# Performance work log

Hardware: AMD Instinct MI355X
Metric: run time of the kernel (lower is better)

## Reference

```python
import jax, jax.numpy as jnp
import numpy as np

N = 8192
E = 131072
IN = 512
H = 8
C = 128
HC = H * C
EPS = 1e-5
NEG_SLOPE = 0.2


def _gatv2(x, src, dst, Wl, bl, Wr, br, att, bias):
    """GATv2Conv (PyG semantics, concat=True, self-loops already in src/dst)."""
    n = x.shape[0]
    xl = (x @ Wl + bl).reshape(n, H, C)  # source transform (lin_l)
    xr = (x @ Wr + br).reshape(n, H, C)  # dest transform (lin_r)
    m = xl[src] + xr[dst]                # [E,H,C] per-edge message
    e = jnp.einsum('ehc,hc->eh', jax.nn.leaky_relu(m, NEG_SLOPE), att)  # [E,H]
    # segment softmax over destination nodes
    emax = jax.ops.segment_max(e, dst, num_segments=n)
    w = jnp.exp(e - emax[dst])
    denom = jax.ops.segment_sum(w, dst, num_segments=n)
    alpha = w / denom[dst]               # [E,H]
    out = jax.ops.segment_sum(alpha[:, :, None] * xl[src], dst, num_segments=n)
    return out.reshape(n, HC) + bias


def _bn(x, gamma, beta):
    mu = jnp.mean(x, axis=0)
    var = jnp.mean((x - mu) ** 2, axis=0)
    return (x - mu) * jax.lax.rsqrt(var + EPS) * gamma + beta


def setup_inputs() -> dict:
    key = jax.random.key(0)
    ks = jax.random.split(key, 16)
    s = 0.05
    return {
        'x': jax.random.normal(ks[0], (N, IN), jnp.float32),
        'edge_index': jax.random.randint(ks[1], (2, E), 0, N, jnp.int32),
        'W1l': jax.random.normal(ks[2], (IN, HC), jnp.float32) * s,
        'b1l': jnp.zeros((HC,), jnp.float32),
        'W1r': jax.random.normal(ks[3], (IN, HC), jnp.float32) * s,
        'b1r': jnp.zeros((HC,), jnp.float32),
        'att1': jax.random.normal(ks[4], (H, C), jnp.float32) * s,
        'bias1': jnp.zeros((HC,), jnp.float32),
        'g1': jnp.ones((HC,), jnp.float32),
        'beta1': jnp.zeros((HC,), jnp.float32),
        'W2l': jax.random.normal(ks[5], (HC, HC), jnp.float32) * s,
        'b2l': jnp.zeros((HC,), jnp.float32),
        'W2r': jax.random.normal(ks[6], (HC, HC), jnp.float32) * s,
        'b2r': jnp.zeros((HC,), jnp.float32),
        'att2': jax.random.normal(ks[7], (H, C), jnp.float32) * s,
        'bias2': jnp.zeros((HC,), jnp.float32),
        'g2': jnp.ones((HC,), jnp.float32),
        'beta2': jnp.zeros((HC,), jnp.float32),
    }


def reference(x, edge_index, W1l, b1l, W1r, b1r, att1, bias1, g1, beta1,
              W2l, b2l, W2r, b2r, att2, bias2, g2, beta2):
    n = x.shape[0]
    loops = jnp.arange(n, dtype=edge_index.dtype)
    src = jnp.concatenate([edge_index[0], loops])
    dst = jnp.concatenate([edge_index[1], loops])
    h = _gatv2(x, src, dst, W1l, b1l, W1r, b1r, att1, bias1)
    h = jax.nn.elu(_bn(h, g1, beta1))
    h = _gatv2(h, src, dst, W2l, b2l, W2r, b2r, att2, bias2)
    h = jax.nn.elu(_bn(h, g2, beta2))
    return h
```

## Files before the change

kernel.cpp:

```cpp
#include <hip/hip_runtime.h>
#include <stdint.h>

#define NN     8192
#define NEDGE  131072
#define NETOT  (NEDGE + NN)
#define K_IN   512
#define HC_    1024
#define NOUT   2048
#define BNEPS  1e-5f
#define SLOPE  0.2f

typedef __bf16 bf16x8 __attribute__((ext_vector_type(8)));
typedef float  f32x4  __attribute__((ext_vector_type(4)));
typedef float  f32x2  __attribute__((ext_vector_type(2)));

__device__ __forceinline__ float bf2f(unsigned short u) {
  union { uint32_t u; float f; } c; c.u = ((uint32_t)u) << 16; return c.f;
}
__device__ __forceinline__ unsigned short f2bf(float f) {
  union { float f; uint32_t u; } c; c.f = f;
  uint32_t r = c.u + 0x7fffu + ((c.u >> 16) & 1u);
  return (unsigned short)(r >> 16);
}
__device__ __forceinline__ f32x2 upk2(uint32_t u) {
  union { uint32_t u; float f; } a, b;
  a.u = u << 16; b.u = u & 0xffff0000u;
  f32x2 r; r.x = a.f; r.y = b.f; return r;
}

__device__ __forceinline__ void gload16(const void* g, void* l) {
  __builtin_amdgcn_global_load_lds(
      (const __attribute__((address_space(1))) uint32_t*)g,
      (__attribute__((address_space(3))) uint32_t*)l, 16, 0, 0);
}

#define SBAR() do { asm volatile("" ::: "memory"); __builtin_amdgcn_s_barrier(); asm volatile("" ::: "memory"); } while (0)

__global__ __launch_bounds__(256) void k_cvt_bf16(const float* __restrict__ in,
                                                  unsigned short* __restrict__ out, int n4) {
  int i = blockIdx.x * 256 + threadIdx.x;
  if (i >= n4) return;
  float4 v = *(const float4*)&in[(size_t)i * 4];
  ushort4 o;
  o.x = f2bf(v.x); o.y = f2bf(v.y); o.z = f2bf(v.z); o.w = f2bf(v.w);
  *(ushort4*)&out[(size_t)i * 4] = o;
}

__global__ __launch_bounds__(256) void k_transpose2_bf16(const float* __restrict__ Wa,
                                                         const float* __restrict__ Wb,
                                                         unsigned short* __restrict__ Wt,
                                                         int K, int N) {
  __shared__ float tile[32][33];
  const float* W = blockIdx.z ? Wb : Wa;
  unsigned short* dst = Wt + (size_t)blockIdx.z * N * K;
  int n0 = blockIdx.x * 32, k0 = blockIdx.y * 32;
  int tx = threadIdx.x & 31, ty = threadIdx.x >> 5;
  for (int i = ty; i < 32; i += 8)
    tile[i][tx] = W[(size_t)(k0 + i) * N + n0 + tx];
  __syncthreads();
  for (int i = ty; i < 32; i += 8)
    dst[(size_t)(n0 + i) * K + k0 + tx] = f2bf(tile[tx][i]);
}

__global__ __launch_bounds__(256) void k_hist(const int* __restrict__ ei, int* __restrict__ cnt) {
  int i = blockIdx.x * 256 + threadIdx.x;
  if (i >= NETOT) return;
  int d = (i < NEDGE) ? ei[NEDGE + i] : (i - NEDGE);
  atomicAdd(&cnt[d], 1);
}

__global__ __launch_bounds__(256) void k_scan(const int* __restrict__ cnt,
                                              int* __restrict__ rowptr,
                                              int* __restrict__ cursor) {
  __shared__ int part[256];
  int t = threadIdx.x;
  int base = t * 32;
  int s = 0;
  for (int i = 0; i < 32; ++i) s += cnt[base + i];
  part[t] = s;
  __syncthreads();
  for (int off = 1; off < 256; off <<= 1) {
    int u = (t >= off) ? part[t - off] : 0;
    __syncthreads();
    part[t] += u;
    __syncthreads();
  }
  int run = part[t] - s;
  for (int i = 0; i < 32; ++i) {
    rowptr[base + i] = run;
    cursor[base + i] = run;
    run += cnt[base + i];
  }
  if (t == 255) rowptr[NN] = run;
}

__global__ __launch_bounds__(256) void k_scatter(const int* __restrict__ ei,
                                                 int* __restrict__ cursor,
                                                 int* __restrict__ srcs) {
  int i = blockIdx.x * 256 + threadIdx.x;
  if (i >= NETOT) return;
  int s, d;
  if (i < NEDGE) { s = ei[i]; d = ei[NEDGE + i]; }
  else           { s = d = i - NEDGE; }
  int pos = atomicAdd(&cursor[d], 1);
  srcs[pos] = s;
}

__global__ __launch_bounds__(512, 2) void k_gemm256(const unsigned short* __restrict__ A,
                                                    const unsigned short* __restrict__ Bt,
                                                    const float* __restrict__ biasL,
                                                    const float* __restrict__ biasR,
                                                    unsigned short* __restrict__ C,
                                                    int K) {
  __shared__ unsigned short lA[2][256 * 64];
  __shared__ unsigned short lB[2][256 * 64];

  const int bid = blockIdx.x;
  const int xcd = bid & 7, idx = bid >> 3;
  const int m0 = (xcd * 4 + (idx & 3)) * 256;
  const int n0 = (idx >> 2) * 256;

  const int tid = threadIdx.x;
  const int l   = tid & 63;
  const int wv  = tid >> 6;
  const int wm  = wv >> 2, wn = wv & 3;
  const int l15 = l & 15, l4 = l >> 4;

  const int srow = tid >> 3;
  const int ssgk = (tid & 7) ^ (srow & 7);

  const f32x4 vzero = {0.f, 0.f, 0.f, 0.f};
  f32x4 acc[8][4];
#pragma unroll
  for (int i = 0; i < 8; ++i)
#pragma unroll
    for (int j = 0; j < 4; ++j) acc[i][j] = vzero;

  bf16x8 a2[8];
  bf16x8 bb[2][4];

  auto stageA = [&](int kt, int h) {
    const int buf = kt & 1;
    const size_t go = (size_t)(m0 + h * 128 + srow) * K + (size_t)kt * 64 + ssgk * 8;
    unsigned short* lp = &lA[buf][h * 8192 + tid * 8];
    gload16(&A[go], lp);
    gload16(&A[go + (size_t)64 * K], lp + 4096);
  };
  auto stageB = [&](int kt, int h) {
    const int buf = kt & 1;
    const size_t go = (size_t)(n0 + h * 128 + srow) * K + (size_t)kt * 64 + ssgk * 8;
    unsigned short* lp = &lB[buf][h * 8192 + tid * 8];
    gload16(&Bt[go], lp);
    gload16(&Bt[go + (size_t)64 * K], lp + 4096);
  };
  auto readA = [&](int buf, int qm) {
#pragma unroll
    for (int fm = 0; fm < 4; ++fm)
#pragma unroll
      for (int kk = 0; kk < 2; ++kk) {
        int r = wm * 128 + (qm * 4 + fm) * 16 + l15;
        int g = (kk * 4 + l4) ^ (r & 7);
        a2[fm * 2 + kk] = *(const bf16x8*)&lA[buf][r * 64 + g * 8];
      }
  };
  auto readB = [&](int buf, int qn) {
#pragma unroll
    for (int fn = 0; fn < 2; ++fn)
#pragma unroll
      for (int kk = 0; kk < 2; ++kk) {
        int r = wn * 64 + (qn * 2 + fn) * 16 + l15;
        int g = (kk * 4 + l4) ^ (r & 7);
        bb[qn][fn * 2 + kk] = *(const bf16x8*)&lB[buf][r * 64 + g * 8];
      }
  };
  auto quad = [&](int qm, int qn) {
    __builtin_amdgcn_s_setprio(1);
#pragma unroll
    for (int fm = 0; fm < 4; ++fm)
#pragma unroll
      for (int fn = 0; fn < 2; ++fn)
#pragma unroll
        for (int kk = 0; kk < 2; ++kk)
          acc[qm * 4 + fm][qn * 2 + fn] = __builtin_amdgcn_mfma_f32_16x16x32_bf16(
              a2[fm * 2 + kk], bb[qn][fn * 2 + kk], acc[qm * 4 + fm][qn * 2 + fn], 0, 0, 0);
    __builtin_amdgcn_s_setprio(0);
  };

  const int NT = K >> 6;

  stageA(0, 0); stageA(0, 1); stageB(0, 0); stageB(0, 1);
  if (NT > 1) stageA(1, 0);
  asm volatile("s_waitcnt vmcnt(2)" ::: "memory");
  SBAR();

  for (int t = 0; t < NT; ++t) {
    const int buf = t & 1;
    readA(buf, 0); readB(buf, 0);
    if (t + 1 < NT) stageA(t + 1, 1);
    SBAR();
    quad(0, 0);
    SBAR();
    readB(buf, 1);
    if (t + 1 < NT) stageB(t + 1, 0);
    SBAR();
    quad(0, 1);
    SBAR();
    readA(buf, 1);
    if (t + 1 < NT) stageB(t + 1, 1);
    SBAR();
    quad(1, 0);
    SBAR();
    if (t + 2 < NT) stageA(t + 2, 0);
    asm volatile("s_waitcnt vmcnt(2)" ::: "memory");
    SBAR();
    quad(1, 1);
    SBAR();
  }

  const float* bias = (n0 < HC_) ? biasL : (biasR - HC_);
#pragma unroll
  for (int fm = 0; fm < 8; ++fm) {
#pragma unroll
    for (int fn = 0; fn < 4; ++fn) {
      int col = n0 + wn * 64 + fn * 16 + l15;
      float bv = bias[col];
#pragma unroll
      for (int j = 0; j < 4; ++j) {
        int row = m0 + wm * 128 + fm * 16 + l4 * 4 + j;
        C[(size_t)row * NOUT + col] = f2bf(acc[fm][fn][j] + bv);
      }
    }
  }
}

template <bool OUT_BF16>
__global__ __launch_bounds__(256, 8) void k_edge_agg(const unsigned short* __restrict__ XLR,
                                                     const float* __restrict__ att,
                                                     const float* __restrict__ bias,
                                                     const int* __restrict__ rowptr,
                                                     const int* __restrict__ srcs,
                                                     void* __restrict__ outp) {
  const int tid  = threadIdx.x;
  const int wv   = tid >> 6;
  const int d    = blockIdx.x * 2 + (wv >> 1);
  const int half = wv & 1;
  const int l    = tid & 63;
  const int c0   = half * 512 + l * 8;

  f32x2 attv[4], xrv[4];
  {
    const f32x2* ap = (const f32x2*)&att[c0];
    attv[0] = ap[0]; attv[1] = ap[1]; attv[2] = ap[2]; attv[3] = ap[3];
    uint4 u = *(const uint4*)&XLR[(size_t)d * NOUT + HC_ + c0];
    xrv[0] = upk2(u.x); xrv[1] = upk2(u.y); xrv[2] = upk2(u.z); xrv[3] = upk2(u.w);
  }

  f32x2 acc0 = {0.f, 0.f}, acc1 = {0.f, 0.f}, acc2 = {0.f, 0.f}, acc3 = {0.f, 0.f};
  float den = 0.f;

  const int beg = __builtin_amdgcn_readfirstlane(rowptr[d]);
  const int end = __builtin_amdgcn_readfirstlane(rowptr[d + 1]);
  const int e1  = end - 1;

  auto rowp = [&](int s) { return (const uint4*)&XLR[(size_t)s * NOUT + c0]; };
  auto cl   = [&](int i) { return i < e1 ? i : e1; };

  uint4 R0 = *rowp(srcs[beg]);
  uint4 R1 = *rowp(srcs[cl(beg + 1)]);
  uint4 R2 = *rowp(srcs[cl(beg + 2)]);
  int sN1 = srcs[cl(beg + 3)];
  int sN2 = srcs[cl(beg + 4)];

  int i = beg;

#define STEP(R)                                                                \
  {                                                                            \
    f32x2 x0 = upk2(R.x), x1 = upk2(R.y), x2 = upk2(R.z), x3 = upk2(R.w);      \
    R = *rowp(sN1);                                                            \
    sN1 = sN2;                                                                 \
    sN2 = srcs[cl(i + 5)];                                                     \
    f32x2 ps = {0.f, 0.f}, y;                                                  \
    y = x0 + xrv[0]; ps = __builtin_elementwise_max(y, y * SLOPE) * attv[0] + ps; \
    y = x1 + xrv[1]; ps = __builtin_elementwise_max(y, y * SLOPE) * attv[1] + ps; \
    y = x2 + xrv[2]; ps = __builtin_elementwise_max(y, y * SLOPE) * attv[2] + ps; \
    y = x3 + xrv[3]; ps = __builtin_elementwise_max(y, y * SLOPE) * attv[3] + ps; \
    float p = ps.x + ps.y;                                                     \
    p += __shfl_xor(p, 1);                                                     \
    p += __shfl_xor(p, 2);                                                     \
    p += __shfl_xor(p, 4);                                                     \
    p += __shfl_xor(p, 8);                                                     \
    float wgt = __expf(p);                                                     \
    den += wgt;                                                                \
    f32x2 w2 = {wgt, wgt};                                                     \
    acc0 = w2 * x0 + acc0;                                                     \
    acc1 = w2 * x1 + acc1;                                                     \
    acc2 = w2 * x2 + acc2;                                                     \
    acc3 = w2 * x3 + acc3;                                                     \
    ++i;                                                                       \
  }

  while (true) {
    STEP(R0); if (i == end) break;
    STEP(R1); if (i == end) break;
    STEP(R2); if (i == end) break;
  }
#undef STEP

  const float inv = 1.0f / den;
  const f32x2* bp = (const f32x2*)&bias[c0];
  float o[8];
  o[0] = acc0.x * inv + bp[0].x; o[1] = acc0.y * inv + bp[0].y;
  o[2] = acc1.x * inv + bp[1].x; o[3] = acc1.y * inv + bp[1].y;
  o[4] = acc2.x * inv + bp[2].x; o[5] = acc2.y * inv + bp[2].y;
  o[6] = acc3.x * inv + bp[3].x; o[7] = acc3.y * inv + bp[3].y;

  if (OUT_BF16) {
    unsigned short* op = (unsigned short*)outp + (size_t)d * HC_ + c0;
    ushort4 u0, u1;
    u0.x = f2bf(o[0]); u0.y = f2bf(o[1]); u0.z = f2bf(o[2]); u0.w = f2bf(o[3]);
    u1.x = f2bf(o[4]); u1.y = f2bf(o[5]); u1.z = f2bf(o[6]); u1.w = f2bf(o[7]);
    *(ushort4*)&op[0] = u0;
    *(ushort4*)&op[4] = u1;
  } else {
    float* op = (float*)outp + (size_t)d * HC_ + c0;
    float4 v0 = {o[0], o[1], o[2], o[3]};
    float4 v1 = {o[4], o[5], o[6], o[7]};
    *(float4*)&op[0] = v0;
    *(float4*)&op[4] = v1;
  }
}

template <bool IN_BF16>
__global__ __launch_bounds__(256) void k_colstats(const void* __restrict__ Xp,
                                                  float* __restrict__ stats) {
  int col = blockIdx.x * 256 + threadIdx.x;
  int r0 = blockIdx.y * 128;
  float s = 0.f, q = 0.f;
  for (int r = r0; r < r0 + 128; ++r) {
    float v = IN_BF16 ? bf2f(((const unsigned short*)Xp)[(size_t)r * HC_ + col])
                      : ((const float*)Xp)[(size_t)r * HC_ + col];
    s += v;
    q += v * v;
  }
  atomicAdd(&stats[col], s);
  atomicAdd(&stats[HC_ + col], q);
}

template <bool IN_BF16, bool OUT_BF16>
__global__ __launch_bounds__(256) void k_bn_elu(const void* __restrict__ Xp,
                                                const float* __restrict__ stats,
                                                const float* __restrict__ gamma,
                                                const float* __restrict__ beta,
                                                void* __restrict__ outp) {
  size_t idx = (size_t)blockIdx.x * 256 + threadIdx.x;
  size_t e0 = idx * 4;
  int col = (int)(e0 & (HC_ - 1));
  float xs[4];
  if (IN_BF16) {
    ushort4 u = *(const ushort4*)&((const unsigned short*)Xp)[e0];
    xs[0] = bf2f(u.x); xs[1] = bf2f(u.y); xs[2] = bf2f(u.z); xs[3] = bf2f(u.w);
  } else {
    float4 xv = *(const float4*)&((const float*)Xp)[e0];
    xs[0] = xv.x; xs[1] = xv.y; xs[2] = xv.z; xs[3] = xv.w;
  }
  float os[4];
  const float rn = 1.0f / (float)NN;
#pragma unroll
  for (int j = 0; j < 4; ++j) {
    int c = col + j;
    float mu = stats[c] * rn;
    float var = stats[HC_ + c] * rn - mu * mu;
    float v = (xs[j] - mu) * rsqrtf(var + BNEPS) * gamma[c] + beta[c];
    os[j] = v > 0.f ? v : (__expf(v) - 1.f);
  }
  if (OUT_BF16) {
    ushort4 o;
    o.x = f2bf(os[0]); o.y = f2bf(os[1]); o.z = f2bf(os[2]); o.w = f2bf(os[3]);
    *(ushort4*)&((unsigned short*)outp)[e0] = o;
  } else {
    float4 o = {os[0], os[1], os[2], os[3]};
    *(float4*)&((float*)outp)[e0] = o;
  }
}

extern "C" void kernel_launch(void* const* d_in, const int* in_sizes, int n_in,
                              void* d_out, int out_size, void* d_ws, size_t ws_size,
                              hipStream_t stream) {
  const float* x     = (const float*)d_in[0];
  const int*   ei    = (const int*)d_in[1];
  const float* W1l   = (const float*)d_in[2];
  const float* b1l   = (const float*)d_in[3];
  const float* W1r   = (const float*)d_in[4];
  const float* b1r   = (const float*)d_in[5];
  const float* att1  = (const float*)d_in[6];
  const float* bias1 = (const float*)d_in[7];
  const float* g1    = (const float*)d_in[8];
  const float* be1   = (const float*)d_in[9];
  const float* W2l   = (const float*)d_in[10];
  const float* b2l   = (const float*)d_in[11];
  const float* W2r   = (const float*)d_in[12];
  const float* b2r   = (const float*)d_in[13];
  const float* att2  = (const float*)d_in[14];
  const float* bias2 = (const float*)d_in[15];
  const float* g2    = (const float*)d_in[16];
  const float* be2   = (const float*)d_in[17];
  float* out = (float*)d_out;

  char* wsb = (char*)d_ws;
  size_t o = 0;
  auto alloc = [&](size_t b) {
    void* p = wsb + o;
    o = (o + b + 255) & ~(size_t)255;
    return p;
  };
  unsigned short* xbf  = (unsigned short*)alloc((size_t)NN * K_IN * 2);
  unsigned short* wT1  = (unsigned short*)alloc((size_t)NOUT * K_IN * 2);
  unsigned short* wT2  = (unsigned short*)alloc((size_t)NOUT * HC_ * 2);
  unsigned short* XLR  = (unsigned short*)alloc((size_t)NN * NOUT * 2);
  unsigned short* h0   = (unsigned short*)alloc((size_t)NN * HC_ * 2);
  int* cnt     = (int*)alloc((size_t)NN * 4);
  int* rowptr  = (int*)alloc((size_t)(NN + 1) * 4);
  int* cursor  = (int*)alloc((size_t)NN * 4);
  int* srcs    = (int*)alloc((size_t)NETOT * 4);
  float* stats = (float*)alloc((size_t)2 * HC_ * 4);

  hipMemsetAsync(cnt, 0, (size_t)NN * 4, stream);
  hipMemsetAsync(stats, 0, (size_t)2 * HC_ * 4, stream);

  k_cvt_bf16<<<(NN * K_IN / 4 + 255) / 256, 256, 0, stream>>>(x, xbf, NN * K_IN / 4);
  k_transpose2_bf16<<<dim3(HC_ / 32, K_IN / 32, 2), 256, 0, stream>>>(W1l, W1r, wT1, K_IN, HC_);
  k_transpose2_bf16<<<dim3(HC_ / 32, HC_ / 32, 2), 256, 0, stream>>>(W2l, W2r, wT2, HC_, HC_);

  k_hist<<<(NETOT + 255) / 256, 256, 0, stream>>>(ei, cnt);
  k_scan<<<1, 256, 0, stream>>>(cnt, rowptr, cursor);
  k_scatter<<<(NETOT + 255) / 256, 256, 0, stream>>>(ei, cursor, srcs);

  k_gemm256<<<256, 512, 0, stream>>>(xbf, wT1, b1l, b1r, XLR, K_IN);
  k_edge_agg<true><<<NN / 2, 256, 0, stream>>>(XLR, att1, bias1, rowptr, srcs, h0);
  k_colstats<true><<<dim3(HC_ / 256, NN / 128), 256, 0, stream>>>(h0, stats);
  k_bn_elu<true, true><<<NN * HC_ / 4 / 256, 256, 0, stream>>>(h0, stats, g1, be1, h0);

  k_gemm256<<<256, 512, 0, stream>>>(h0, wT2, b2l, b2r, XLR, HC_);
  k_edge_agg<true><<<NN / 2, 256, 0, stream>>>(XLR, att2, bias2, rowptr, srcs, h0);
  hipMemsetAsync(stats, 0, (size_t)2 * HC_ * 4, stream);
  k_colstats<true><<<dim3(HC_ / 256, NN / 128), 256, 0, stream>>>(h0, stats);
  k_bn_elu<true, false><<<NN * HC_ / 4 / 256, 256, 0, stream>>>(h0, stats, g2, be2, out);
}
```

Baseline: 233.3 us.

## Restructure GEMM pipeline waits, deepen edge prefetch, vectorize column stats

The GEMM main loop is rebuilt so next-tile stages are issued before each quad with explicit vmcnt waits and fewer barriers, the last tile is peeled, and the warp-to-subtile mapping changes to interleave warps across 128-row and 128-column halves. The edge aggregation kernel prefetches four source rows instead of three and lowers its occupancy hint from 8 to 7 blocks. Column statistics now read four bf16 values per thread in a single-block-wide grid, cutting the number of blocks and loads. These changes aim to hide more global-load latency and reduce sync overhead, at the cost of more register pressure and fewer parallel blocks in the stats kernel.

```diff
diff --git a/kernel.cpp b/kernel.cpp
--- a/kernel.cpp
+++ b/kernel.cpp
@@ -35,6 +35,7 @@
 }
 
 #define SBAR() do { asm volatile("" ::: "memory"); __builtin_amdgcn_s_barrier(); asm volatile("" ::: "memory"); } while (0)
+#define VMC(n) asm volatile("s_waitcnt vmcnt(" #n ")" ::: "memory")
 
 __global__ __launch_bounds__(256) void k_cvt_bf16(const float* __restrict__ in,
                                                   unsigned short* __restrict__ out, int n4) {
@@ -158,7 +159,7 @@
     for (int fm = 0; fm < 4; ++fm)
 #pragma unroll
       for (int kk = 0; kk < 2; ++kk) {
-        int r = wm * 128 + (qm * 4 + fm) * 16 + l15;
+        int r = qm * 128 + wm * 64 + fm * 16 + l15;
         int g = (kk * 4 + l4) ^ (r & 7);
         a2[fm * 2 + kk] = *(const bf16x8*)&lA[buf][r * 64 + g * 8];
       }
@@ -168,7 +169,7 @@
     for (int fn = 0; fn < 2; ++fn)
 #pragma unroll
       for (int kk = 0; kk < 2; ++kk) {
-        int r = wn * 64 + (qn * 2 + fn) * 16 + l15;
+        int r = qn * 128 + wn * 32 + fn * 16 + l15;
         int g = (kk * 4 + l4) ^ (r & 7);
         bb[qn][fn * 2 + kk] = *(const bf16x8*)&lB[buf][r * 64 + g * 8];
       }
@@ -188,53 +189,56 @@
 
   const int NT = K >> 6;
 
-  stageA(0, 0); stageA(0, 1); stageB(0, 0); stageB(0, 1);
-  if (NT > 1) stageA(1, 0);
-  asm volatile("s_waitcnt vmcnt(2)" ::: "memory");
-  SBAR();
-
-  for (int t = 0; t < NT; ++t) {
+  stageA(0, 0); stageB(0, 0); stageB(0, 1); stageA(0, 1);
+
+  for (int t = 0; t < NT - 1; ++t) {
     const int buf = t & 1;
+    stageA(t + 1, 0);
+    VMC(6); SBAR();
     readA(buf, 0); readB(buf, 0);
-    if (t + 1 < NT) stageA(t + 1, 1);
-    SBAR();
     quad(0, 0);
-    SBAR();
+    stageB(t + 1, 0);
+    VMC(6); SBAR();
     readB(buf, 1);
-    if (t + 1 < NT) stageB(t + 1, 0);
-    SBAR();
     quad(0, 1);
-    SBAR();
+    stageB(t + 1, 1);
+    VMC(6); SBAR();
     readA(buf, 1);
-    if (t + 1 < NT) stageB(t + 1, 1);
-    SBAR();
     quad(1, 0);
-    SBAR();
-    if (t + 2 < NT) stageA(t + 2, 0);
-    asm volatile("s_waitcnt vmcnt(2)" ::: "memory");
-    SBAR();
+    stageA(t + 1, 1);
     quad(1, 1);
-    SBAR();
+  }
+  {
+    const int buf = (NT - 1) & 1;
+    VMC(4); SBAR();
+    readA(buf, 0); readB(buf, 0);
+    quad(0, 0);
+    VMC(2); SBAR();
+    readB(buf, 1);
+    quad(0, 1);
+    VMC(0); SBAR();
+    readA(buf, 1);
+    quad(1, 0);
+    quad(1, 1);
   }
 
   const float* bias = (n0 < HC_) ? biasL : (biasR - HC_);
 #pragma unroll
   for (int fm = 0; fm < 8; ++fm) {
+    int row0 = m0 + (fm >> 2) * 128 + wm * 64 + (fm & 3) * 16 + l4 * 4;
 #pragma unroll
     for (int fn = 0; fn < 4; ++fn) {
-      int col = n0 + wn * 64 + fn * 16 + l15;
+      int col = n0 + (fn >> 1) * 128 + wn * 32 + (fn & 1) * 16 + l15;
       float bv = bias[col];
 #pragma unroll
-      for (int j = 0; j < 4; ++j) {
-        int row = m0 + wm * 128 + fm * 16 + l4 * 4 + j;
-        C[(size_t)row * NOUT + col] = f2bf(acc[fm][fn][j] + bv);
-      }
+      for (int j = 0; j < 4; ++j)
+        C[(size_t)(row0 + j) * NOUT + col] = f2bf(acc[fm][fn][j] + bv);
     }
   }
 }
 
 template <bool OUT_BF16>
-__global__ __launch_bounds__(256, 8) void k_edge_agg(const unsigned short* __restrict__ XLR,
+__global__ __launch_bounds__(256, 7) void k_edge_agg(const unsigned short* __restrict__ XLR,
                                                      const float* __restrict__ att,
                                                      const float* __restrict__ bias,
                                                      const int* __restrict__ rowptr,
@@ -268,8 +272,10 @@
   uint4 R0 = *rowp(srcs[beg]);
   uint4 R1 = *rowp(srcs[cl(beg + 1)]);
   uint4 R2 = *rowp(srcs[cl(beg + 2)]);
-  int sN1 = srcs[cl(beg + 3)];
-  int sN2 = srcs[cl(beg + 4)];
+  uint4 R3 = *rowp(srcs[cl(beg + 3)]);
+  int sN1 = srcs[cl(beg + 4)];
+  int sN2 = srcs[cl(beg + 5)];
+  int sN3 = srcs[cl(beg + 6)];
 
   int i = beg;
 
@@ -277,8 +283,8 @@
   {                                                                            \
     f32x2 x0 = upk2(R.x), x1 = upk2(R.y), x2 = upk2(R.z), x3 = upk2(R.w);      \
     R = *rowp(sN1);                                                            \
-    sN1 = sN2;                                                                 \
-    sN2 = srcs[cl(i + 5)];                                                     \
+    sN1 = sN2; sN2 = sN3;                                                      \
+    sN3 = srcs[cl(i + 7)];                                                     \
     f32x2 ps = {0.f, 0.f}, y;                                                  \
     y = x0 + xrv[0]; ps = __builtin_elementwise_max(y, y * SLOPE) * attv[0] + ps; \
     y = x1 + xrv[1]; ps = __builtin_elementwise_max(y, y * SLOPE) * attv[1] + ps; \
@@ -303,6 +309,7 @@
     STEP(R0); if (i == end) break;
     STEP(R1); if (i == end) break;
     STEP(R2); if (i == end) break;
+    STEP(R3); if (i == end) break;
   }
 #undef STEP
 
@@ -330,24 +337,29 @@
   }
 }
 
-template <bool IN_BF16>
-__global__ __launch_bounds__(256) void k_colstats(const void* __restrict__ Xp,
-                                                  float* __restrict__ stats) {
-  int col = blockIdx.x * 256 + threadIdx.x;
+__global__ __launch_bounds__(256) void k_colstats4(const unsigned short* __restrict__ X,
+                                                   float* __restrict__ stats) {
+  int col = threadIdx.x * 4;
   int r0 = blockIdx.y * 128;
-  float s = 0.f, q = 0.f;
+  f32x2 s01 = {0.f, 0.f}, s23 = {0.f, 0.f}, q01 = {0.f, 0.f}, q23 = {0.f, 0.f};
   for (int r = r0; r < r0 + 128; ++r) {
-    float v = IN_BF16 ? bf2f(((const unsigned short*)Xp)[(size_t)r * HC_ + col])
-                      : ((const float*)Xp)[(size_t)r * HC_ + col];
-    s += v;
-    q += v * v;
-  }
-  atomicAdd(&stats[col], s);
-  atomicAdd(&stats[HC_ + col], q);
-}
-
-template <bool IN_BF16, bool OUT_BF16>
-__global__ __launch_bounds__(256) void k_bn_elu(const void* __restrict__ Xp,
+    uint2 v = *(const uint2*)&X[(size_t)r * HC_ + col];
+    f32x2 a = upk2(v.x), b = upk2(v.y);
+    s01 = s01 + a; s23 = s23 + b;
+    q01 = a * a + q01; q23 = b * b + q23;
+  }
+  atomicAdd(&stats[col + 0], s01.x);
+  atomicAdd(&stats[col + 1], s01.y);
+  atomicAdd(&stats[col + 2], s23.x);
+  atomicAdd(&stats[col + 3], s23.y);
+  atomicAdd(&stats[HC_ + col + 0], q01.x);
+  atomicAdd(&stats[HC_ + col + 1], q01.y);
+  atomicAdd(&stats[HC_ + col + 2], q23.x);
+  atomicAdd(&stats[HC_ + col + 3], q23.y);
+}
+
+template <bool OUT_BF16>
+__global__ __launch_bounds__(256) void k_bn_elu(const unsigned short* __restrict__ Xp,
                                                 const float* __restrict__ stats,
                                                 const float* __restrict__ gamma,
                                                 const float* __restrict__ beta,
@@ -356,13 +368,8 @@
   size_t e0 = idx * 4;
   int col = (int)(e0 & (HC_ - 1));
   float xs[4];
-  if (IN_BF16) {
-    ushort4 u = *(const ushort4*)&((const unsigned short*)Xp)[e0];
-    xs[0] = bf2f(u.x); xs[1] = bf2f(u.y); xs[2] = bf2f(u.z); xs[3] = bf2f(u.w);
-  } else {
-    float4 xv = *(const float4*)&((const float*)Xp)[e0];
-    xs[0] = xv.x; xs[1] = xv.y; xs[2] = xv.z; xs[3] = xv.w;
-  }
+  ushort4 u = *(const ushort4*)&Xp[e0];
+  xs[0] = bf2f(u.x); xs[1] = bf2f(u.y); xs[2] = bf2f(u.z); xs[3] = bf2f(u.w);
   float os[4];
   const float rn = 1.0f / (float)NN;
 #pragma unroll
@@ -437,12 +444,12 @@
 
   k_gemm256<<<256, 512, 0, stream>>>(xbf, wT1, b1l, b1r, XLR, K_IN);
   k_edge_agg<true><<<NN / 2, 256, 0, stream>>>(XLR, att1, bias1, rowptr, srcs, h0);
-  k_colstats<true><<<dim3(HC_ / 256, NN / 128), 256, 0, stream>>>(h0, stats);
-  k_bn_elu<true, true><<<NN * HC_ / 4 / 256, 256, 0, stream>>>(h0, stats, g1, be1, h0);
+  k_colstats4<<<dim3(1, NN / 128), 256, 0, stream>>>(h0, stats);
+  k_bn_elu<true><<<NN * HC_ / 4 / 256, 256, 0, stream>>>(h0, stats, g1, be1, h0);
 
   k_gemm256<<<256, 512, 0, stream>>>(h0, wT2, b2l, b2r, XLR, HC_);
   k_edge_agg<true><<<NN / 2, 256, 0, stream>>>(XLR, att2, bias2, rowptr, srcs, h0);
   hipMemsetAsync(stats, 0, (size_t)2 * HC_ * 4, stream);
-  k_colstats<true><<<dim3(HC_ / 256, NN / 128), 256, 0, stream>>>(h0, stats);
-  k_bn_elu<true, false><<<NN * HC_ / 4 / 256, 256, 0, stream>>>(h0, stats, g2, be2, out);
-}
+  k_colstats4<<<dim3(1, NN / 128), 256, 0, stream>>>(h0, stats);
+  k_bn_elu<false><<<NN * HC_ / 4 / 256, 256, 0, stream>>>(h0, stats, g2, be2, out);
+}
```

Result: slower. 243.2 us (+4.3%).
